# Optimization experiments

Measured on AMD Instinct MI355X. Metric: run time of the kernel, lower is better.

Reference implementation:

```python
import jax, jax.numpy as jnp
import numpy as np

N_NODES = 50000
N_EDGES = 600000
N_GRAPHS = 64
HID = 128
NLAYERS = 4
IN_DIM = 5
NCLS = 5
EPS = 1e-5


def setup_inputs() -> dict:
    key = jax.random.key(0)
    ks = jax.random.split(key, 16)
    x = jax.random.normal(ks[0], (N_NODES, IN_DIM), dtype=jnp.float32)
    edge_index = jax.random.randint(ks[1], (2, N_EDGES), 0, N_NODES, dtype=jnp.int64)
    batch = jnp.sort(jax.random.randint(ks[2], (N_NODES,), 0, N_GRAPHS, dtype=jnp.int64))
    s = 0.05
    Wp = jax.random.normal(ks[3], (IN_DIM, HID), jnp.float32) * s
    bp = jnp.zeros((HID,), jnp.float32)
    Wg = jax.random.normal(ks[4], (NLAYERS, HID, HID), jnp.float32) * s
    bg = jnp.zeros((NLAYERS, HID), jnp.float32)
    gamma = jnp.ones((NLAYERS, HID), jnp.float32)
    beta = jnp.zeros((NLAYERS, HID), jnp.float32)
    W1 = jax.random.normal(ks[5], (2 * HID, HID), jnp.float32) * s
    b1 = jnp.zeros((HID,), jnp.float32)
    W2 = jax.random.normal(ks[6], (HID, HID // 2), jnp.float32) * s
    b2 = jnp.zeros((HID // 2,), jnp.float32)
    W3 = jax.random.normal(ks[7], (HID // 2, NCLS), jnp.float32) * s
    b3 = jnp.zeros((NCLS,), jnp.float32)
    return {"x": x, "edge_index": edge_index, "batch": batch, "Wp": Wp, "bp": bp,
            "Wg": Wg, "bg": bg, "gamma": gamma, "beta": beta,
            "W1": W1, "b1": b1, "W2": W2, "b2": b2, "W3": W3, "b3": b3}


def reference(x, edge_index, batch, Wp, bp, Wg, bg, gamma, beta, W1, b1, W2, b2, W3, b3):
    N = x.shape[0]
    # GCN with added self-loops and symmetric normalization (PyG GCNConv defaults)
    loop = jnp.arange(N)
    src = jnp.concatenate([edge_index[0], loop])
    dst = jnp.concatenate([edge_index[1], loop])
    deg = jax.ops.segment_sum(jnp.ones_like(dst, dtype=x.dtype), dst, num_segments=N)
    dinv = jax.lax.rsqrt(deg)  # deg >= 1 thanks to self-loops
    norm = dinv[src] * dinv[dst]  # [E+N]
    h = x @ Wp + bp  # [N, HID]
    for i in range(NLAYERS):
        m = h @ Wg[i]
        agg = jax.ops.segment_sum(m[src] * norm[:, None], dst, num_segments=N) + bg[i]
        # BatchNorm1d (training-mode stats over nodes)
        mu = jnp.mean(agg, axis=0)
        var = jnp.var(agg, axis=0)
        h = gamma[i] * (agg - mu) * jax.lax.rsqrt(var + EPS) + beta[i]
        h = jax.nn.relu(h)  # dropout is identity in eval mode
    # mean_max global pooling per graph
    cnt = jax.ops.segment_sum(jnp.ones((N,), h.dtype), batch, num_segments=N_GRAPHS)
    x_mean = jax.ops.segment_sum(h, batch, num_segments=N_GRAPHS) / jnp.maximum(cnt, 1.0)[:, None]
    x_max = jax.ops.segment_max(h, batch, num_segments=N_GRAPHS)
    x_max = jnp.where(jnp.isfinite(x_max), x_max, 0.0)
    pooled = jnp.concatenate([x_mean, x_max], axis=1)  # [B, 2*HID]
    h1 = jax.nn.relu(pooled @ W1 + b1)
    h2 = jax.nn.relu(h1 @ W2 + b2)
    return h2 @ W3 + b3  # [B, num_classes]
```

## Files before the change

kernel.cpp:

```cpp
#include <hip/hip_runtime.h>
#include <hip/hip_bf16.h>

#define N_NODES 50000
#define N_EDGES 600000
#define N_GRAPHS 64
#define HID 128
#define NLAYERS 4
#define IN_DIM 5
#define NCLS 5
#define EPS 1e-5f
#define SCAN_BLK ((N_NODES + 511) / 512)
#define FILL_BLK ((N_EDGES + 255) / 256)
#define POOL_CHUNKS 16
#define BSLOT 64
#define WS 136

typedef __attribute__((ext_vector_type(8))) short s16x8;
typedef __attribute__((ext_vector_type(4))) float f32x4;

__device__ __forceinline__ unsigned short f2bf(float x) {
    unsigned u = __float_as_uint(x);
    unsigned r = (u + 0x7fffu + ((u >> 16) & 1u)) >> 16;
    return (unsigned short)r;
}
__device__ __forceinline__ float2 bfpair(unsigned u) {
    float2 r;
    r.x = __uint_as_float(u << 16);
    r.y = __uint_as_float(u & 0xffff0000u);
    return r;
}
__device__ __forceinline__ float bf2f(unsigned short s) {
    return __uint_as_float(((unsigned)s) << 16);
}


__global__ void k_count(const int* __restrict__ dst, int* __restrict__ cnt) {
    int i = blockIdx.x * blockDim.x + threadIdx.x;
    if (i < N_EDGES) atomicAdd(&cnt[dst[i]], 1);
}

__global__ void k_scan1(const int* __restrict__ cnt, int* __restrict__ rp, int* __restrict__ bsum) {
    __shared__ int s[512];
    int t = threadIdx.x;
    int i = blockIdx.x * 512 + t;
    int v = (i < N_NODES) ? cnt[i] : 0;
    s[t] = v;
    __syncthreads();
    for (int off = 1; off < 512; off <<= 1) {
        int x = (t >= off) ? s[t - off] : 0;
        __syncthreads();
        s[t] += x;
        __syncthreads();
    }
    if (i < N_NODES) rp[i + 1] = s[t];
    if (t == 511) bsum[blockIdx.x] = s[511];
}

__global__ void k_scan2g(int* __restrict__ bsum, const int* __restrict__ batch,
                         int* __restrict__ gstart) {
    if (blockIdx.x == 0) {
        __shared__ int s[128];
        int t = threadIdx.x;
        int v = (t < SCAN_BLK) ? bsum[t] : 0;
        s[t] = v;
        __syncthreads();
        for (int off = 1; off < 128; off <<= 1) {
            int x = (t >= off) ? s[t - off] : 0;
            __syncthreads();
            s[t] += x;
            __syncthreads();
        }
        if (t < SCAN_BLK) bsum[t] = s[t] - v;
    } else {
        int t = threadIdx.x;
        if (t <= N_GRAPHS) {
            int lo = 0, hi = N_NODES;
            while (lo < hi) {
                int mid = (lo + hi) >> 1;
                if (batch[mid] < t) lo = mid + 1; else hi = mid;
            }
            gstart[t] = lo;
        }
    }
}

__global__ void k_scan3d(int* __restrict__ rp, const int* __restrict__ bsum,
                         const int* __restrict__ cnt, float* __restrict__ dinv) {
    int i = blockIdx.x * 512 + threadIdx.x;
    if (i < N_NODES) {
        rp[i + 1] += bsum[blockIdx.x];
        dinv[i] = rsqrtf((float)(cnt[i] + 1));
    }
    if (i == 0) rp[0] = 0;
}

__global__ void k_fillw(const int* __restrict__ src, const int* __restrict__ dst,
                        const int* __restrict__ rp, int* __restrict__ cursor,
                        int2* __restrict__ cw, const float* __restrict__ dinv,
                        const float* __restrict__ Wg, unsigned short* __restrict__ WtG) {
    int b = blockIdx.x;
    if (b < FILL_BLK) {
        int e = b * 256 + threadIdx.x;
        if (e < N_EDGES) {
            int d = dst[e];
            int pos = atomicAdd(&cursor[d], 1);
            int s = src[e];
            int2 p;
            p.x = s;
            p.y = __float_as_int(dinv[s]);
            cw[rp[d] + pos] = p;
        }
    } else {
        int idx = (b - FILL_BLK) * 256 + threadIdx.x;
        int l = idx >> 14;
        int r = idx & 16383;
        int n = r >> 7, k = r & 127;
        WtG[idx] = f2bf(Wg[l * HID * HID + k * HID + n]);
    }
}


__global__ __launch_bounds__(256, 3) void k_gemmM(const unsigned short* __restrict__ Abf,
                                                  const float* __restrict__ x,
                                                  const float* __restrict__ Wp,
                                                  const float* __restrict__ bp,
                                                  const unsigned short* __restrict__ WtG,
                                                  unsigned short* __restrict__ Bm,
                                                  const float* __restrict__ psum,
                                                  const float* __restrict__ psq,
                                                  const float* __restrict__ gamma,
                                                  const float* __restrict__ beta,
                                                  int layer0) {
    __shared__ unsigned short Wt[HID * WS];
    __shared__ unsigned short Al[64 * WS];
    __shared__ float scl[HID], shf[HID];
    int t = threadIdx.x;
    {
        const uint4* Wg4 = (const uint4*)WtG;
        for (int idx = t; idx < HID * 16; idx += 256) {
            int n = idx >> 4, c = idx & 15;
            *(uint4*)&Wt[n * WS + c * 8] = Wg4[idx];
        }
    }
    if (!layer0 && t < HID) {
        float s = 0.f, s2 = 0.f;
#pragma unroll 8
        for (int b = 0; b < BSLOT; b++) {
            s += psum[b * HID + t];
            s2 += psq[b * HID + t];
        }
        const float invN = 1.f / (float)N_NODES;
        float mu = s * invN;
        float var = s2 * invN - mu * mu;
        float rs = rsqrtf(var + EPS) * gamma[t];
        scl[t] = rs;
        shf[t] = beta[t] - mu * rs;
    }
    int lane = t & 63, wv = t >> 6;
    int rbase = (wv & 1) * 32;
    int cbase = (wv >> 1) * 64;
    int mr = lane & 15, q = lane >> 4;
    const int numTiles = (N_NODES + 63) / 64;
    for (int tile = blockIdx.x; tile < numTiles; tile += gridDim.x) {
        int n0 = tile * 64;
        int limRow = min(64, N_NODES - n0);
        __syncthreads();
        if (layer0) {
            for (int idx = t; idx < 64 * HID; idx += 256) {
                int n = idx >> 7, k = idx & 127;
                int node = n0 + n;
                float acc = 0.f;
                if (node < N_NODES) {
                    acc = bp[k];
#pragma unroll
                    for (int j = 0; j < IN_DIM; j++) acc += x[node * IN_DIM + j] * Wp[j * HID + k];
                }
                Al[n * WS + k] = f2bf(acc);
            }
        } else {
            const uint2* Ag = (const uint2*)(Abf + (size_t)n0 * HID);
            for (int idx = t; idx < 64 * 32; idx += 256) {
                int row = idx >> 5, c4 = idx & 31;
                uint2 u = (row < limRow) ? Ag[row * 32 + c4] : make_uint2(0u, 0u);
                float2 ab = bfpair(u.x);
                float2 cd = bfpair(u.y);
                int kf = c4 * 4;
                float4 sc = *(const float4*)&scl[kf];
                float4 sh = *(const float4*)&shf[kf];
                float v0 = fmaxf(ab.x * sc.x + sh.x, 0.f);
                float v1 = fmaxf(ab.y * sc.y + sh.y, 0.f);
                float v2 = fmaxf(cd.x * sc.z + sh.z, 0.f);
                float v3 = fmaxf(cd.y * sc.w + sh.w, 0.f);
                unsigned lo = (unsigned)f2bf(v0) | ((unsigned)f2bf(v1) << 16);
                unsigned hi = (unsigned)f2bf(v2) | ((unsigned)f2bf(v3) << 16);
                *(uint2*)&Al[row * WS + kf] = make_uint2(lo, hi);
            }
        }
        __syncthreads();
        f32x4 acc[2][4];
#pragma unroll
        for (int rt = 0; rt < 2; rt++)
#pragma unroll
            for (int ct = 0; ct < 4; ct++) acc[rt][ct] = (f32x4){0.f, 0.f, 0.f, 0.f};
#pragma unroll
        for (int kk = 0; kk < HID; kk += 32) {
            s16x8 a0 = *(const s16x8*)&Al[(rbase + mr) * WS + kk + q * 8];
            s16x8 a1 = *(const s16x8*)&Al[(rbase + 16 + mr) * WS + kk + q * 8];
#pragma unroll
            for (int ct = 0; ct < 4; ct++) {
                s16x8 b = *(const s16x8*)&Wt[(cbase + ct * 16 + mr) * WS + kk + q * 8];
                acc[0][ct] = __builtin_amdgcn_mfma_f32_16x16x32_bf16(a0, b, acc[0][ct], 0, 0, 0);
                acc[1][ct] = __builtin_amdgcn_mfma_f32_16x16x32_bf16(a1, b, acc[1][ct], 0, 0, 0);
            }
        }
        __syncthreads();
#pragma unroll
        for (int rt = 0; rt < 2; rt++)
#pragma unroll
            for (int ct = 0; ct < 4; ct++)
#pragma unroll
                for (int r = 0; r < 4; r++) {
                    int rloc = rbase + rt * 16 + q * 4 + r;
                    int f = cbase + ct * 16 + mr;
                    Al[rloc * WS + f] = f2bf(acc[rt][ct][r]);
                }
        __syncthreads();
        for (int idx = t; idx < 64 * 16; idx += 256) {
            int row = idx >> 4, c = idx & 15;
            if (row < limRow)
                *(uint4*)&Bm[(size_t)(n0 + row) * HID + c * 8] = *(const uint4*)&Al[row * WS + c * 8];
        }
    }
}


__global__ __launch_bounds__(256) void k_gather(const uint4* __restrict__ Bm4,
                                                const int* __restrict__ rp,
                                                const int2* __restrict__ cw,
                                                const float* __restrict__ dinv,
                                                const float* __restrict__ bg,
                                                unsigned short* __restrict__ Aout,
                                                float* __restrict__ psum,
                                                float* __restrict__ psq) {
    __shared__ float ls[4 * HID], lq[4 * HID];
    int wave = threadIdx.x >> 6;
    int lane = threadIdx.x & 63;
    int s = lane & 15;
    int p = lane >> 4;
    int f = s * 8;
    float ts0 = 0.f, ts1 = 0.f, ts2 = 0.f, ts3 = 0.f, ts4 = 0.f, ts5 = 0.f, ts6 = 0.f, ts7 = 0.f;
    float tq0 = 0.f, tq1 = 0.f, tq2 = 0.f, tq3 = 0.f, tq4 = 0.f, tq5 = 0.f, tq6 = 0.f, tq7 = 0.f;
#pragma unroll 1
    for (int it = 0; it < 4; it++) {
        int v = blockIdx.x * 16 + wave * 4 + it;
        int beg = rp[v], end = rp[v + 1];
        float dv = dinv[v];
        float a0 = 0.f, a1 = 0.f, a2 = 0.f, a3 = 0.f, a4 = 0.f, a5 = 0.f, a6 = 0.f, a7 = 0.f;
        if (p == 0) {
            uint4 u = Bm4[(size_t)v * 16 + s];
            float2 q0 = bfpair(u.x), q1 = bfpair(u.y), q2 = bfpair(u.z), q3 = bfpair(u.w);
            a0 = q0.x * dv; a1 = q0.y * dv; a2 = q1.x * dv; a3 = q1.y * dv;
            a4 = q2.x * dv; a5 = q2.y * dv; a6 = q3.x * dv; a7 = q3.y * dv;
        }
        int e = beg + p;
        for (; e + 4 < end; e += 8) {
            int2 pe0 = cw[e];
            int2 pe1 = cw[e + 4];
            uint4 u0 = Bm4[(size_t)pe0.x * 16 + s];
            uint4 u1 = Bm4[(size_t)pe1.x * 16 + s];
            float w0 = __int_as_float(pe0.y);
            float w1 = __int_as_float(pe1.y);
            float2 x0 = bfpair(u0.x), x1 = bfpair(u0.y), x2 = bfpair(u0.z), x3 = bfpair(u0.w);
            float2 y0 = bfpair(u1.x), y1 = bfpair(u1.y), y2 = bfpair(u1.z), y3 = bfpair(u1.w);
            a0 += x0.x * w0 + y0.x * w1;
            a1 += x0.y * w0 + y0.y * w1;
            a2 += x1.x * w0 + y1.x * w1;
            a3 += x1.y * w0 + y1.y * w1;
            a4 += x2.x * w0 + y2.x * w1;
            a5 += x2.y * w0 + y2.y * w1;
            a6 += x3.x * w0 + y3.x * w1;
            a7 += x3.y * w0 + y3.y * w1;
        }
        if (e < end) {
            int2 pe = cw[e];
            uint4 u = Bm4[(size_t)pe.x * 16 + s];
            float w = __int_as_float(pe.y);
            float2 x0 = bfpair(u.x), x1 = bfpair(u.y), x2 = bfpair(u.z), x3 = bfpair(u.w);
            a0 += x0.x * w; a1 += x0.y * w; a2 += x1.x * w; a3 += x1.y * w;
            a4 += x2.x * w; a5 += x2.y * w; a6 += x3.x * w; a7 += x3.y * w;
        }
        a0 += __shfl_xor(a0, 16); a1 += __shfl_xor(a1, 16);
        a2 += __shfl_xor(a2, 16); a3 += __shfl_xor(a3, 16);
        a4 += __shfl_xor(a4, 16); a5 += __shfl_xor(a5, 16);
        a6 += __shfl_xor(a6, 16); a7 += __shfl_xor(a7, 16);
        a0 += __shfl_xor(a0, 32); a1 += __shfl_xor(a1, 32);
        a2 += __shfl_xor(a2, 32); a3 += __shfl_xor(a3, 32);
        a4 += __shfl_xor(a4, 32); a5 += __shfl_xor(a5, 32);
        a6 += __shfl_xor(a6, 32); a7 += __shfl_xor(a7, 32);
        if (p == 0) {
            float r0 = a0 * dv + bg[f + 0];
            float r1 = a1 * dv + bg[f + 1];
            float r2 = a2 * dv + bg[f + 2];
            float r3 = a3 * dv + bg[f + 3];
            float r4 = a4 * dv + bg[f + 4];
            float r5 = a5 * dv + bg[f + 5];
            float r6 = a6 * dv + bg[f + 6];
            float r7 = a7 * dv + bg[f + 7];
            unsigned short b0 = f2bf(r0), b1 = f2bf(r1), b2 = f2bf(r2), b3 = f2bf(r3);
            unsigned short b4 = f2bf(r4), b5 = f2bf(r5), b6 = f2bf(r6), b7 = f2bf(r7);
            uint4 o;
            o.x = (unsigned)b0 | ((unsigned)b1 << 16);
            o.y = (unsigned)b2 | ((unsigned)b3 << 16);
            o.z = (unsigned)b4 | ((unsigned)b5 << 16);
            o.w = (unsigned)b6 | ((unsigned)b7 << 16);
            *(uint4*)&Aout[(size_t)v * HID + f] = o;
            float v0 = bf2f(b0), v1 = bf2f(b1), v2 = bf2f(b2), v3 = bf2f(b3);
            float v4 = bf2f(b4), v5 = bf2f(b5), v6 = bf2f(b6), v7 = bf2f(b7);
            ts0 += v0; ts1 += v1; ts2 += v2; ts3 += v3;
            ts4 += v4; ts5 += v5; ts6 += v6; ts7 += v7;
            tq0 += v0 * v0; tq1 += v1 * v1; tq2 += v2 * v2; tq3 += v3 * v3;
            tq4 += v4 * v4; tq5 += v5 * v5; tq6 += v6 * v6; tq7 += v7 * v7;
        }
    }
    if (p == 0) {
        float* lsw = &ls[wave * HID + f];
        float* lqw = &lq[wave * HID + f];
        lsw[0] = ts0; lsw[1] = ts1; lsw[2] = ts2; lsw[3] = ts3;
        lsw[4] = ts4; lsw[5] = ts5; lsw[6] = ts6; lsw[7] = ts7;
        lqw[0] = tq0; lqw[1] = tq1; lqw[2] = tq2; lqw[3] = tq3;
        lqw[4] = tq4; lqw[5] = tq5; lqw[6] = tq6; lqw[7] = tq7;
    }
    __syncthreads();
    int tt = threadIdx.x;
    if (tt < HID) {
        float ssum = ls[tt] + ls[HID + tt] + ls[2 * HID + tt] + ls[3 * HID + tt];
        float ssq = lq[tt] + lq[HID + tt] + lq[2 * HID + tt] + lq[3 * HID + tt];
        int slot = blockIdx.x & (BSLOT - 1);
        atomicAdd(&psum[slot * HID + tt], ssum);
        atomicAdd(&psq[slot * HID + tt], ssq);
    }
}


__global__ __launch_bounds__(128) void k_pool(const unsigned short* __restrict__ A,
                                              const float* __restrict__ psum,
                                              const float* __restrict__ psq,
                                              const float* __restrict__ gamma,
                                              const float* __restrict__ beta,
                                              const int* __restrict__ gstart,
                                              float* __restrict__ poolPart) {
    int g = blockIdx.x;
    int c = blockIdx.y;
    int f = threadIdx.x;
    float s = 0.f, s2 = 0.f;
#pragma unroll 8
    for (int b = 0; b < BSLOT; b++) {
        s += psum[b * HID + f];
        s2 += psq[b * HID + f];
    }
    const float invN = 1.f / (float)N_NODES;
    float mu = s * invN;
    float var = s2 * invN - mu * mu;
    float sc = rsqrtf(var + EPS) * gamma[f];
    float sh = beta[f] - mu * sc;
    int beg = gstart[g], end = gstart[g + 1];
    int len = end - beg;
    int per = (len + POOL_CHUNKS - 1) / POOL_CHUNKS;
    int s0 = beg + c * per;
    int s1 = min(s0 + per, end);
    float sa = 0.f, sb = 0.f, ma = 0.f, mb = 0.f;
    int n = s0;
    for (; n + 1 < s1; n += 2) {
        float v0 = bf2f(A[(size_t)n * HID + f]);
        float v1 = bf2f(A[(size_t)(n + 1) * HID + f]);
        v0 = fmaxf(v0 * sc + sh, 0.f);
        v1 = fmaxf(v1 * sc + sh, 0.f);
        sa += v0; ma = fmaxf(ma, v0);
        sb += v1; mb = fmaxf(mb, v1);
    }
    if (n < s1) {
        float v = fmaxf(bf2f(A[(size_t)n * HID + f]) * sc + sh, 0.f);
        sa += v; ma = fmaxf(ma, v);
    }
    poolPart[((size_t)g * POOL_CHUNKS + c) * 256 + f] = sa + sb;
    poolPart[((size_t)g * POOL_CHUNKS + c) * 256 + 128 + f] = fmaxf(ma, mb);
}


__global__ __launch_bounds__(128) void k_head(const float* __restrict__ poolPart,
                                              const int* __restrict__ gstart,
                                              const float* __restrict__ W1, const float* __restrict__ b1,
                                              const float* __restrict__ W2, const float* __restrict__ b2,
                                              const float* __restrict__ W3, const float* __restrict__ b3,
                                              float* __restrict__ out) {
    __shared__ float pl[2 * HID];
    __shared__ float h1[HID];
    __shared__ float h2[HID / 2];
    int g = blockIdx.x, t = threadIdx.x;
    float cnt = fmaxf((float)(gstart[g + 1] - gstart[g]), 1.f);
    float s = 0.f, mx = 0.f;
#pragma unroll
    for (int c = 0; c < POOL_CHUNKS; c++) {
        const float* p = &poolPart[((size_t)g * POOL_CHUNKS + c) * 256];
        s += p[t];
        mx = fmaxf(mx, p[128 + t]);
    }
    pl[t] = s / cnt;
    pl[HID + t] = mx;
    __syncthreads();
    float acc = b1[t];
    for (int k = 0; k < 2 * HID; k++) acc += pl[k] * W1[k * HID + t];
    h1[t] = fmaxf(acc, 0.f);
    __syncthreads();
    if (t < HID / 2) {
        float a2 = b2[t];
        for (int k = 0; k < HID; k++) a2 += h1[k] * W2[k * (HID / 2) + t];
        h2[t] = fmaxf(a2, 0.f);
    }
    __syncthreads();
    if (t < NCLS) {
        float a3 = b3[t];
        for (int k = 0; k < HID / 2; k++) a3 += h2[k] * W3[k * NCLS + t];
        out[g * NCLS + t] = a3;
    }
}

extern "C" void kernel_launch(void* const* d_in, const int* in_sizes, int n_in,
                              void* d_out, int out_size, void* d_ws, size_t ws_size,
                              hipStream_t stream) {
    const float* x     = (const float*)d_in[0];
    const int*   ei    = (const int*)d_in[1];
    const int*   batch = (const int*)d_in[2];
    const float* Wp    = (const float*)d_in[3];
    const float* bp    = (const float*)d_in[4];
    const float* Wg    = (const float*)d_in[5];
    const float* bg    = (const float*)d_in[6];
    const float* gamma = (const float*)d_in[7];
    const float* beta  = (const float*)d_in[8];
    const float* W1    = (const float*)d_in[9];
    const float* b1    = (const float*)d_in[10];
    const float* W2    = (const float*)d_in[11];
    const float* b2    = (const float*)d_in[12];
    const float* W3    = (const float*)d_in[13];
    const float* b3    = (const float*)d_in[14];
    const int* src = ei;
    const int* dst = ei + N_EDGES;
    float* out = (float*)d_out;

    char* base = (char*)d_ws;
    size_t off = 0;
    auto alloc = [&](size_t bytes) -> void* {
        void* p = base + off;
        off += (bytes + 255) & ~(size_t)255;
        return p;
    };
    int*   counts = (int*)alloc((size_t)N_NODES * 4);
    int*   cursor = (int*)alloc((size_t)N_NODES * 4);
    float* psum   = (float*)alloc((size_t)NLAYERS * BSLOT * HID * 4);
    float* psq    = (float*)alloc((size_t)NLAYERS * BSLOT * HID * 4);
    size_t zeroBytes = off;
    int*   rp      = (int*)alloc((size_t)(N_NODES + 1) * 4);
    int*   bsum    = (int*)alloc(128 * 4);
    int2*  cw      = (int2*)alloc((size_t)N_EDGES * 8);
    float* dinv    = (float*)alloc((size_t)N_NODES * 4);
    int*   gstart  = (int*)alloc((size_t)(N_GRAPHS + 1) * 4);
    float* poolPart= (float*)alloc((size_t)N_GRAPHS * POOL_CHUNKS * 256 * 4);
    unsigned short* WtG = (unsigned short*)alloc((size_t)NLAYERS * HID * HID * 2);
    unsigned short* A = (unsigned short*)alloc((size_t)N_NODES * HID * 2);
    unsigned short* B = (unsigned short*)alloc((size_t)N_NODES * HID * 2);
    (void)ws_size; (void)in_sizes; (void)n_in; (void)out_size;

    hipMemsetAsync(d_ws, 0, zeroBytes, stream);

    k_count<<<(N_EDGES + 255) / 256, 256, 0, stream>>>(dst, counts);
    k_scan1<<<SCAN_BLK, 512, 0, stream>>>(counts, rp, bsum);
    k_scan2g<<<2, 128, 0, stream>>>(bsum, batch, gstart);
    k_scan3d<<<SCAN_BLK, 512, 0, stream>>>(rp, bsum, counts, dinv);
    k_fillw<<<FILL_BLK + (NLAYERS * HID * HID) / 256, 256, 0, stream>>>(
        src, dst, rp, cursor, cw, dinv, Wg, WtG);

    for (int i = 0; i < NLAYERS; i++) {
        int pl = (i == 0) ? 0 : (i - 1);
        k_gemmM<<<768, 256, 0, stream>>>(A, x, Wp, bp, WtG + (size_t)i * HID * HID, B,
                                         psum + (size_t)pl * BSLOT * HID,
                                         psq + (size_t)pl * BSLOT * HID,
                                         gamma + pl * HID, beta + pl * HID,
                                         (i == 0) ? 1 : 0);
        k_gather<<<N_NODES / 16, 256, 0, stream>>>((const uint4*)B, rp, cw, dinv,
                                                   bg + i * HID, A,
                                                   psum + (size_t)i * BSLOT * HID,
                                                   psq + (size_t)i * BSLOT * HID);
    }
    dim3 pg(N_GRAPHS, POOL_CHUNKS);
    k_pool<<<pg, 128, 0, stream>>>(A, psum + (size_t)3 * BSLOT * HID,
                                   psq + (size_t)3 * BSLOT * HID,
                                   gamma + 3 * HID, beta + 3 * HID, gstart, poolPart);
    k_head<<<N_GRAPHS, 128, 0, stream>>>(poolPart, gstart, W1, b1, W2, b2, W3, b3, out);
}
```

Baseline: 386.8 us.

## Map one node per quarter-wave in GCN gather instead of splitting edges

The gather kernel used to process four nodes in turn per wave, with the four 16-lane groups splitting each node's edge list and combining through cross-lane shuffles. Now each 16-lane group handles its own node and walks that node's whole edge list, so the per-node shuffle reduction and the serial four-step node loop go away. The shuffles move to the BatchNorm statistics, which are reduced once per wave. The cost is load imbalance: groups whose nodes have higher degree make the whole wave wait, and each lane now issues a longer dependent chain of loads.

Measured after the change: 379.1 us. 1.02x faster.

```diff
diff --git a/kernel.cpp b/kernel.cpp
--- a/kernel.cpp
+++ b/kernel.cpp
@@ -248,80 +248,81 @@
     int s = lane & 15;
     int p = lane >> 4;
     int f = s * 8;
-    float ts0 = 0.f, ts1 = 0.f, ts2 = 0.f, ts3 = 0.f, ts4 = 0.f, ts5 = 0.f, ts6 = 0.f, ts7 = 0.f;
-    float tq0 = 0.f, tq1 = 0.f, tq2 = 0.f, tq3 = 0.f, tq4 = 0.f, tq5 = 0.f, tq6 = 0.f, tq7 = 0.f;
-#pragma unroll 1
-    for (int it = 0; it < 4; it++) {
-        int v = blockIdx.x * 16 + wave * 4 + it;
-        int beg = rp[v], end = rp[v + 1];
-        float dv = dinv[v];
-        float a0 = 0.f, a1 = 0.f, a2 = 0.f, a3 = 0.f, a4 = 0.f, a5 = 0.f, a6 = 0.f, a7 = 0.f;
-        if (p == 0) {
-            uint4 u = Bm4[(size_t)v * 16 + s];
-            float2 q0 = bfpair(u.x), q1 = bfpair(u.y), q2 = bfpair(u.z), q3 = bfpair(u.w);
-            a0 = q0.x * dv; a1 = q0.y * dv; a2 = q1.x * dv; a3 = q1.y * dv;
-            a4 = q2.x * dv; a5 = q2.y * dv; a6 = q3.x * dv; a7 = q3.y * dv;
-        }
-        int e = beg + p;
-        for (; e + 4 < end; e += 8) {
-            int2 pe0 = cw[e];
-            int2 pe1 = cw[e + 4];
-            uint4 u0 = Bm4[(size_t)pe0.x * 16 + s];
-            uint4 u1 = Bm4[(size_t)pe1.x * 16 + s];
-            float w0 = __int_as_float(pe0.y);
-            float w1 = __int_as_float(pe1.y);
-            float2 x0 = bfpair(u0.x), x1 = bfpair(u0.y), x2 = bfpair(u0.z), x3 = bfpair(u0.w);
-            float2 y0 = bfpair(u1.x), y1 = bfpair(u1.y), y2 = bfpair(u1.z), y3 = bfpair(u1.w);
-            a0 += x0.x * w0 + y0.x * w1;
-            a1 += x0.y * w0 + y0.y * w1;
-            a2 += x1.x * w0 + y1.x * w1;
-            a3 += x1.y * w0 + y1.y * w1;
-            a4 += x2.x * w0 + y2.x * w1;
-            a5 += x2.y * w0 + y2.y * w1;
-            a6 += x3.x * w0 + y3.x * w1;
-            a7 += x3.y * w0 + y3.y * w1;
-        }
-        if (e < end) {
-            int2 pe = cw[e];
-            uint4 u = Bm4[(size_t)pe.x * 16 + s];
-            float w = __int_as_float(pe.y);
-            float2 x0 = bfpair(u.x), x1 = bfpair(u.y), x2 = bfpair(u.z), x3 = bfpair(u.w);
-            a0 += x0.x * w; a1 += x0.y * w; a2 += x1.x * w; a3 += x1.y * w;
-            a4 += x2.x * w; a5 += x2.y * w; a6 += x3.x * w; a7 += x3.y * w;
-        }
-        a0 += __shfl_xor(a0, 16); a1 += __shfl_xor(a1, 16);
-        a2 += __shfl_xor(a2, 16); a3 += __shfl_xor(a3, 16);
-        a4 += __shfl_xor(a4, 16); a5 += __shfl_xor(a5, 16);
-        a6 += __shfl_xor(a6, 16); a7 += __shfl_xor(a7, 16);
-        a0 += __shfl_xor(a0, 32); a1 += __shfl_xor(a1, 32);
-        a2 += __shfl_xor(a2, 32); a3 += __shfl_xor(a3, 32);
-        a4 += __shfl_xor(a4, 32); a5 += __shfl_xor(a5, 32);
-        a6 += __shfl_xor(a6, 32); a7 += __shfl_xor(a7, 32);
-        if (p == 0) {
-            float r0 = a0 * dv + bg[f + 0];
-            float r1 = a1 * dv + bg[f + 1];
-            float r2 = a2 * dv + bg[f + 2];
-            float r3 = a3 * dv + bg[f + 3];
-            float r4 = a4 * dv + bg[f + 4];
-            float r5 = a5 * dv + bg[f + 5];
-            float r6 = a6 * dv + bg[f + 6];
-            float r7 = a7 * dv + bg[f + 7];
-            unsigned short b0 = f2bf(r0), b1 = f2bf(r1), b2 = f2bf(r2), b3 = f2bf(r3);
-            unsigned short b4 = f2bf(r4), b5 = f2bf(r5), b6 = f2bf(r6), b7 = f2bf(r7);
-            uint4 o;
-            o.x = (unsigned)b0 | ((unsigned)b1 << 16);
-            o.y = (unsigned)b2 | ((unsigned)b3 << 16);
-            o.z = (unsigned)b4 | ((unsigned)b5 << 16);
-            o.w = (unsigned)b6 | ((unsigned)b7 << 16);
-            *(uint4*)&Aout[(size_t)v * HID + f] = o;
-            float v0 = bf2f(b0), v1 = bf2f(b1), v2 = bf2f(b2), v3 = bf2f(b3);
-            float v4 = bf2f(b4), v5 = bf2f(b5), v6 = bf2f(b6), v7 = bf2f(b7);
-            ts0 += v0; ts1 += v1; ts2 += v2; ts3 += v3;
-            ts4 += v4; ts5 += v5; ts6 += v6; ts7 += v7;
-            tq0 += v0 * v0; tq1 += v1 * v1; tq2 += v2 * v2; tq3 += v3 * v3;
-            tq4 += v4 * v4; tq5 += v5 * v5; tq6 += v6 * v6; tq7 += v7 * v7;
-        }
-    }
+    int v = blockIdx.x * 16 + wave * 4 + p;
+    int beg = rp[v], end = rp[v + 1];
+    float dv = dinv[v];
+    float a0, a1, a2, a3, a4, a5, a6, a7;
+    {
+        uint4 u = Bm4[(size_t)v * 16 + s];
+        float2 q0 = bfpair(u.x), q1 = bfpair(u.y), q2 = bfpair(u.z), q3 = bfpair(u.w);
+        a0 = q0.x * dv; a1 = q0.y * dv; a2 = q1.x * dv; a3 = q1.y * dv;
+        a4 = q2.x * dv; a5 = q2.y * dv; a6 = q3.x * dv; a7 = q3.y * dv;
+    }
+    int e = beg;
+    for (; e + 1 < end; e += 2) {
+        int2 pe0 = cw[e];
+        int2 pe1 = cw[e + 1];
+        uint4 u0 = Bm4[(size_t)pe0.x * 16 + s];
+        uint4 u1 = Bm4[(size_t)pe1.x * 16 + s];
+        float w0 = __int_as_float(pe0.y);
+        float w1 = __int_as_float(pe1.y);
+        float2 x0 = bfpair(u0.x), x1 = bfpair(u0.y), x2 = bfpair(u0.z), x3 = bfpair(u0.w);
+        float2 y0 = bfpair(u1.x), y1 = bfpair(u1.y), y2 = bfpair(u1.z), y3 = bfpair(u1.w);
+        a0 += x0.x * w0 + y0.x * w1;
+        a1 += x0.y * w0 + y0.y * w1;
+        a2 += x1.x * w0 + y1.x * w1;
+        a3 += x1.y * w0 + y1.y * w1;
+        a4 += x2.x * w0 + y2.x * w1;
+        a5 += x2.y * w0 + y2.y * w1;
+        a6 += x3.x * w0 + y3.x * w1;
+        a7 += x3.y * w0 + y3.y * w1;
+    }
+    if (e < end) {
+        int2 pe = cw[e];
+        uint4 u = Bm4[(size_t)pe.x * 16 + s];
+        float w = __int_as_float(pe.y);
+        float2 x0 = bfpair(u.x), x1 = bfpair(u.y), x2 = bfpair(u.z), x3 = bfpair(u.w);
+        a0 += x0.x * w; a1 += x0.y * w; a2 += x1.x * w; a3 += x1.y * w;
+        a4 += x2.x * w; a5 += x2.y * w; a6 += x3.x * w; a7 += x3.y * w;
+    }
+    float r0 = a0 * dv + bg[f + 0];
+    float r1 = a1 * dv + bg[f + 1];
+    float r2 = a2 * dv + bg[f + 2];
+    float r3 = a3 * dv + bg[f + 3];
+    float r4 = a4 * dv + bg[f + 4];
+    float r5 = a5 * dv + bg[f + 5];
+    float r6 = a6 * dv + bg[f + 6];
+    float r7 = a7 * dv + bg[f + 7];
+    unsigned short b0 = f2bf(r0), b1 = f2bf(r1), b2 = f2bf(r2), b3 = f2bf(r3);
+    unsigned short b4 = f2bf(r4), b5 = f2bf(r5), b6 = f2bf(r6), b7 = f2bf(r7);
+    uint4 o;
+    o.x = (unsigned)b0 | ((unsigned)b1 << 16);
+    o.y = (unsigned)b2 | ((unsigned)b3 << 16);
+    o.z = (unsigned)b4 | ((unsigned)b5 << 16);
+    o.w = (unsigned)b6 | ((unsigned)b7 << 16);
+    *(uint4*)&Aout[(size_t)v * HID + f] = o;
+    float v0 = bf2f(b0), v1 = bf2f(b1), v2 = bf2f(b2), v3 = bf2f(b3);
+    float v4 = bf2f(b4), v5 = bf2f(b5), v6 = bf2f(b6), v7 = bf2f(b7);
+    float ts0 = v0, ts1 = v1, ts2 = v2, ts3 = v3;
+    float ts4 = v4, ts5 = v5, ts6 = v6, ts7 = v7;
+    float tq0 = v0 * v0, tq1 = v1 * v1, tq2 = v2 * v2, tq3 = v3 * v3;
+    float tq4 = v4 * v4, tq5 = v5 * v5, tq6 = v6 * v6, tq7 = v7 * v7;
+    ts0 += __shfl_xor(ts0, 16); ts1 += __shfl_xor(ts1, 16);
+    ts2 += __shfl_xor(ts2, 16); ts3 += __shfl_xor(ts3, 16);
+    ts4 += __shfl_xor(ts4, 16); ts5 += __shfl_xor(ts5, 16);
+    ts6 += __shfl_xor(ts6, 16); ts7 += __shfl_xor(ts7, 16);
+    tq0 += __shfl_xor(tq0, 16); tq1 += __shfl_xor(tq1, 16);
+    tq2 += __shfl_xor(tq2, 16); tq3 += __shfl_xor(tq3, 16);
+    tq4 += __shfl_xor(tq4, 16); tq5 += __shfl_xor(tq5, 16);
+    tq6 += __shfl_xor(tq6, 16); tq7 += __shfl_xor(tq7, 16);
+    ts0 += __shfl_xor(ts0, 32); ts1 += __shfl_xor(ts1, 32);
+    ts2 += __shfl_xor(ts2, 32); ts3 += __shfl_xor(ts3, 32);
+    ts4 += __shfl_xor(ts4, 32); ts5 += __shfl_xor(ts5, 32);
+    ts6 += __shfl_xor(ts6, 32); ts7 += __shfl_xor(ts7, 32);
+    tq0 += __shfl_xor(tq0, 32); tq1 += __shfl_xor(tq1, 32);
+    tq2 += __shfl_xor(tq2, 32); tq3 += __shfl_xor(tq3, 32);
+    tq4 += __shfl_xor(tq4, 32); tq5 += __shfl_xor(tq5, 32);
+    tq6 += __shfl_xor(tq6, 32); tq7 += __shfl_xor(tq7, 32);
     if (p == 0) {
         float* lsw = &ls[wave * HID + f];
         float* lqw = &lq[wave * HID + f];
```
